# Performance work log

Hardware: AMD Instinct MI355X
Metric: run time of the kernel (lower is better)

Reference implementation:

```python
import jax, jax.numpy as jnp
import numpy as np

M = 65536  # total flattened feature length (sum of ragged segment lengths n_k)
K = 4096   # number of segments (sub-networks)
B = 256    # batch size


def setup_inputs() -> dict:
    key = jax.random.key(0)
    k1, k2, k3 = jax.random.split(key, 3)
    x = jax.random.normal(k1, (B, 1, M), dtype=jnp.float32)
    w = jax.random.normal(k2, (M,), dtype=jnp.float32)
    # contiguous ragged segments: sorted segment ids in [0, K)
    seg_ids = jnp.sort(jax.random.randint(k3, (M,), 0, K, dtype=jnp.int32))
    return {"x": x, "w": w, "seg_ids": seg_ids, "num_segments": K}


def reference(x, w, seg_ids, num_segments):
    # GINN input layer: for each batch row, slice the flat input into K ragged
    # contiguous segments, dot each segment with the matching slice of the flat
    # weight vector, concatenate the K scalars, apply tanh.
    # Equivalent fused form: u2[b,k] = sum_{i in seg k} w[i]*x[b,0,i]; out = tanh(u2)
    xs = x[:, 0, :]                      # [B, M]
    prod = xs * w                        # [B, M] elementwise
    seg_sum = jax.vmap(
        lambda p: jax.ops.segment_sum(p, seg_ids, num_segments=num_segments)
    )(prod)                              # [B, K]
    return jnp.tanh(seg_sum)
```

## Files before the change

kernel.cpp:

```cpp
#include <hip/hip_runtime.h>


#define TPB   256
#define WIN   1024
#define EPL   16
#define SLOTS 192
#define ITERS 4

__global__ __launch_bounds__(TPB) void zero_out_k(float* __restrict__ out, int n4) {
    int i = blockIdx.x * blockDim.x + threadIdx.x;
    if (i < n4) reinterpret_cast<float4*>(out)[i] = make_float4(0.f, 0.f, 0.f, 0.f);
}

__global__ __launch_bounds__(TPB) void seg_persist(
        const float* __restrict__ x,
        const float* __restrict__ w,
        const int*   __restrict__ ids,
        float* __restrict__ out,
        float* __restrict__ carry,
        int M, int K, int NW, int B) {
    __shared__ float slab[TPB / 64][2][SLOTS];

    const int ln  = threadIdx.x & 63;
    const int wv  = threadIdx.x >> 6;
    const int wid = blockIdx.x * (TPB / 64) + wv;
    const int win = wid % NW;
    const int grp = wid / NW;
    const int bp0 = grp * ITERS;
    const size_t mbase = (size_t)win * WIN + (size_t)ln * EPL;
    const int halfB = B / 2;

    const int4*   id4 = reinterpret_cast<const int4*>(ids + mbase);
    const float4* w4  = reinterpret_cast<const float4*>(w + mbase);
    int4   i0 = id4[0], i1 = id4[1], i2 = id4[2], i3 = id4[3];
    float4 q0 = w4[0],  q1 = w4[1],  q2 = w4[2],  q3 = w4[3];

    const int firstId = __shfl(i0.x, 0);
    const int lastId  = __shfl(i3.w, 63);
    const int span    = min(lastId - firstId + 1, SLOTS);

    float* __restrict__ sA = slab[wv][0];
    float* __restrict__ sB = slab[wv][1];

    float4 aC[4], cC[4], aN[4], cN[4];
    {
        const float4* xa4 = reinterpret_cast<const float4*>(x + (size_t)bp0 * M + mbase);
        const float4* xb4 = reinterpret_cast<const float4*>(x + (size_t)(bp0 + halfB) * M + mbase);
        aC[0] = xa4[0]; aC[1] = xa4[1]; aC[2] = xa4[2]; aC[3] = xa4[3];
        cC[0] = xb4[0]; cC[1] = xb4[1]; cC[2] = xb4[2]; cC[3] = xb4[3];
    }

    #pragma unroll
    for (int it = 0; it < ITERS; ++it) {
        const int bp  = bp0 + it;
        const int bpn = bp0 + ((it + 1 < ITERS) ? (it + 1) : it);
        {
            const float4* xa4 = reinterpret_cast<const float4*>(x + (size_t)bpn * M + mbase);
            const float4* xb4 = reinterpret_cast<const float4*>(x + (size_t)(bpn + halfB) * M + mbase);
            aN[0] = xa4[0]; aN[1] = xa4[1]; aN[2] = xa4[2]; aN[3] = xa4[3];
            cN[0] = xb4[0]; cN[1] = xb4[1]; cN[2] = xb4[2]; cN[3] = xb4[3];
        }
        #pragma unroll
        for (int i = ln; i < 2 * SLOTS; i += 64) (&sA[0])[i] = 0.f;
        asm volatile("s_waitcnt lgkmcnt(0)" ::: "memory");
        __builtin_amdgcn_sched_barrier(0);

        float accA = 0.f, accB = 0.f;
        int prev = i0.x;
        #define STEP(idv, xav, xbv, wvv)                               \
            if ((idv) != prev) {                                       \
                int s = min(prev - firstId, SLOTS - 1);                \
                atomicAdd(&sA[s], accA);                               \
                atomicAdd(&sB[s], accB);                               \
                accA = 0.f; accB = 0.f; prev = (idv);                  \
            }                                                          \
            accA = fmaf((xav), (wvv), accA);                           \
            accB = fmaf((xbv), (wvv), accB);

        STEP(i0.x, aC[0].x, cC[0].x, q0.x)  STEP(i0.y, aC[0].y, cC[0].y, q0.y)
        STEP(i0.z, aC[0].z, cC[0].z, q0.z)  STEP(i0.w, aC[0].w, cC[0].w, q0.w)
        STEP(i1.x, aC[1].x, cC[1].x, q1.x)  STEP(i1.y, aC[1].y, cC[1].y, q1.y)
        STEP(i1.z, aC[1].z, cC[1].z, q1.z)  STEP(i1.w, aC[1].w, cC[1].w, q1.w)
        STEP(i2.x, aC[2].x, cC[2].x, q2.x)  STEP(i2.y, aC[2].y, cC[2].y, q2.y)
        STEP(i2.z, aC[2].z, cC[2].z, q2.z)  STEP(i2.w, aC[2].w, cC[2].w, q2.w)
        STEP(i3.x, aC[3].x, cC[3].x, q3.x)  STEP(i3.y, aC[3].y, cC[3].y, q3.y)
        STEP(i3.z, aC[3].z, cC[3].z, q3.z)  STEP(i3.w, aC[3].w, cC[3].w, q3.w)
        #undef STEP
        {
            int s = min(prev - firstId, SLOTS - 1);
            atomicAdd(&sA[s], accA);
            atomicAdd(&sB[s], accB);
        }
        asm volatile("s_waitcnt lgkmcnt(0)" ::: "memory");
        __builtin_amdgcn_sched_barrier(0);

        for (int i = ln; i < 2 * span; i += 64) {
            int rr  = (i >= span) ? 1 : 0;
            int s   = i - rr * span;
            int id  = firstId + s;
            int row = rr ? (bp + halfB) : bp;
            float v = slab[wv][rr][s];
            if (s == 0)
                carry[((size_t)row * NW + win) * 2 + 0] = v;
            else if (id == lastId)
                carry[((size_t)row * NW + win) * 2 + 1] = v;
            else
                out[(size_t)row * K + id] = tanhf(v);
        }
        asm volatile("s_waitcnt lgkmcnt(0)" ::: "memory");
        __builtin_amdgcn_sched_barrier(0);

        #pragma unroll
        for (int j = 0; j < 4; ++j) { aC[j] = aN[j]; cC[j] = cN[j]; }
    }
}

__global__ __launch_bounds__(TPB) void seg_fixup(
        const int*   __restrict__ ids,
        const float* __restrict__ carry,
        float* __restrict__ out,
        int K, int NW, int B) {
    int t = blockIdx.x * blockDim.x + threadIdx.x;
    if (t >= B * NW) return;
    int row = t / NW;
    int win = t - row * NW;

    int firstId = ids[win * WIN];
    int lastId  = ids[win * WIN + WIN - 1];
    float cF = carry[((size_t)row * NW + win) * 2 + 0];
    float cL = carry[((size_t)row * NW + win) * 2 + 1];

    int prevLast = (win > 0) ? ids[win * WIN - 1] : -1;
    if (prevLast != firstId)
        out[(size_t)row * K + firstId] = tanhf(cF);

    float tot = cL;
    if (win + 1 < NW) {
        int nextFirst = ids[(win + 1) * WIN];
        if (nextFirst == lastId)
            tot += carry[((size_t)row * NW + win + 1) * 2 + 0];
    }
    out[(size_t)row * K + lastId] = tanhf(tot);
}

extern "C" void kernel_launch(void* const* d_in, const int* in_sizes, int n_in,
                              void* d_out, int out_size, void* d_ws, size_t ws_size,
                              hipStream_t stream) {
    const float* x       = (const float*)d_in[0];
    const float* w       = (const float*)d_in[1];
    const int*   seg_ids = (const int*)d_in[2];
    float* out = (float*)d_out;

    const int M = in_sizes[1];
    const int B = in_sizes[0] / M;
    const int K = out_size / B;
    const int NW = M / WIN;

    float* carry = (float*)d_ws;

    const int n4 = out_size / 4;
    zero_out_k<<<(n4 + TPB - 1) / TPB, TPB, 0, stream>>>(out, n4);

    const int nwaves = NW * ((B / 2) / ITERS);
    const int nblk   = nwaves / (TPB / 64);
    seg_persist<<<nblk, TPB, 0, stream>>>(x, w, seg_ids, out, carry, M, K, NW, B);

    const int nfix = B * NW;
    seg_fixup<<<(nfix + TPB - 1) / TPB, TPB, 0, stream>>>(seg_ids, carry, out, K, NW, B);
}
```

Measured before the change: 31.24 us.

## Stage x through LDS with direct global-to-LDS loads and drop zero kernel

Replaces the persistent per-wave kernel, which prefetched x into registers over four iterations, with a 2D grid of one block per window and eight batch rows. x is copied straight into LDS using global_load_lds, and each wave reduces two rows. The separate output-zeroing kernel is removed; the fixup kernel now zeroes the empty segment ids between windows instead. This saves a launch and register pressure, but loses the cross-iteration prefetch overlap and reloads ids and w in every block.

```diff
diff --git a/kernel.cpp b/kernel.cpp
--- a/kernel.cpp
+++ b/kernel.cpp
@@ -3,115 +3,113 @@
 
 #define TPB   256
 #define WIN   1024
-#define EPL   16
+#define ROWS  8
 #define SLOTS 192
-#define ITERS 4
 
-__global__ __launch_bounds__(TPB) void zero_out_k(float* __restrict__ out, int n4) {
-    int i = blockIdx.x * blockDim.x + threadIdx.x;
-    if (i < n4) reinterpret_cast<float4*>(out)[i] = make_float4(0.f, 0.f, 0.f, 0.f);
+__device__ __forceinline__ void gload_lds16(const float* g, void* l) {
+    __builtin_amdgcn_global_load_lds(
+        (const __attribute__((address_space(1))) void*)g,
+        (__attribute__((address_space(3)))  void*)l,
+        16, 0, 0);
 }
 
-__global__ __launch_bounds__(TPB) void seg_persist(
+__global__ __launch_bounds__(TPB) void seg_glds(
         const float* __restrict__ x,
         const float* __restrict__ w,
         const int*   __restrict__ ids,
         float* __restrict__ out,
         float* __restrict__ carry,
-        int M, int K, int NW, int B) {
-    __shared__ float slab[TPB / 64][2][SLOTS];
+        int M, int K, int NW) {
+    __shared__ float4 xstage[ROWS][WIN / 4];
+    __shared__ float  slab[ROWS][SLOTS];
 
-    const int ln  = threadIdx.x & 63;
-    const int wv  = threadIdx.x >> 6;
-    const int wid = blockIdx.x * (TPB / 64) + wv;
-    const int win = wid % NW;
-    const int grp = wid / NW;
-    const int bp0 = grp * ITERS;
-    const size_t mbase = (size_t)win * WIN + (size_t)ln * EPL;
-    const int halfB = B / 2;
+    const int ln   = threadIdx.x & 63;
+    const int wv   = threadIdx.x >> 6;
+    const int win  = blockIdx.x;
+    const int r0   = blockIdx.y * ROWS;
+    const int rowA = r0 + 2 * wv;
+    const int rowB = rowA + 1;
+    const int fb   = win * WIN + ln * 4;
 
-    const int4*   id4 = reinterpret_cast<const int4*>(ids + mbase);
-    const float4* w4  = reinterpret_cast<const float4*>(w + mbase);
-    int4   i0 = id4[0], i1 = id4[1], i2 = id4[2], i3 = id4[3];
-    float4 q0 = w4[0],  q1 = w4[1],  q2 = w4[2],  q3 = w4[3];
+    const float* ga = x + (size_t)rowA * M + fb;
+    const float* gb = x + (size_t)rowB * M + fb;
+    #pragma unroll
+    for (int j = 0; j < 4; ++j)
+        gload_lds16(ga + j * 256, (void*)&xstage[2 * wv + 0][j * 64]);
+    #pragma unroll
+    for (int j = 0; j < 4; ++j)
+        gload_lds16(gb + j * 256, (void*)&xstage[2 * wv + 1][j * 64]);
+
+    int4   i0 = *reinterpret_cast<const int4*>(ids + fb);
+    int4   i1 = *reinterpret_cast<const int4*>(ids + fb + 256);
+    int4   i2 = *reinterpret_cast<const int4*>(ids + fb + 512);
+    int4   i3 = *reinterpret_cast<const int4*>(ids + fb + 768);
+    float4 q0 = *reinterpret_cast<const float4*>(w + fb);
+    float4 q1 = *reinterpret_cast<const float4*>(w + fb + 256);
+    float4 q2 = *reinterpret_cast<const float4*>(w + fb + 512);
+    float4 q3 = *reinterpret_cast<const float4*>(w + fb + 768);
+
+    #pragma unroll
+    for (int i = ln; i < 2 * SLOTS; i += 64)
+        (&slab[2 * wv][0])[i] = 0.f;
+
+    asm volatile("s_waitcnt vmcnt(0) lgkmcnt(0)" ::: "memory");
+    __builtin_amdgcn_sched_barrier(0);
 
     const int firstId = __shfl(i0.x, 0);
     const int lastId  = __shfl(i3.w, 63);
     const int span    = min(lastId - firstId + 1, SLOTS);
 
-    float* __restrict__ sA = slab[wv][0];
-    float* __restrict__ sB = slab[wv][1];
-
-    float4 aC[4], cC[4], aN[4], cN[4];
-    {
-        const float4* xa4 = reinterpret_cast<const float4*>(x + (size_t)bp0 * M + mbase);
-        const float4* xb4 = reinterpret_cast<const float4*>(x + (size_t)(bp0 + halfB) * M + mbase);
-        aC[0] = xa4[0]; aC[1] = xa4[1]; aC[2] = xa4[2]; aC[3] = xa4[3];
-        cC[0] = xb4[0]; cC[1] = xb4[1]; cC[2] = xb4[2]; cC[3] = xb4[3];
+    #pragma unroll
+    for (int rr = 0; rr < 2; ++rr) {
+        float* __restrict__ sl = slab[2 * wv + rr];
+        float acc = 0.f;
+        int prev = i0.x;
+        #define STEP(idv, xv, wvv)                                     \
+            if ((idv) != prev) {                                       \
+                atomicAdd(&sl[min(prev - firstId, SLOTS - 1)], acc);   \
+                acc = 0.f; prev = (idv);                               \
+            }                                                          \
+            acc = fmaf((xv), (wvv), acc);
+        {
+            float4 xq = xstage[2 * wv + rr][0 * 64 + ln];
+            STEP(i0.x, xq.x, q0.x) STEP(i0.y, xq.y, q0.y)
+            STEP(i0.z, xq.z, q0.z) STEP(i0.w, xq.w, q0.w)
+        }
+        {
+            float4 xq = xstage[2 * wv + rr][1 * 64 + ln];
+            STEP(i1.x, xq.x, q1.x) STEP(i1.y, xq.y, q1.y)
+            STEP(i1.z, xq.z, q1.z) STEP(i1.w, xq.w, q1.w)
+        }
+        {
+            float4 xq = xstage[2 * wv + rr][2 * 64 + ln];
+            STEP(i2.x, xq.x, q2.x) STEP(i2.y, xq.y, q2.y)
+            STEP(i2.z, xq.z, q2.z) STEP(i2.w, xq.w, q2.w)
+        }
+        {
+            float4 xq = xstage[2 * wv + rr][3 * 64 + ln];
+            STEP(i3.x, xq.x, q3.x) STEP(i3.y, xq.y, q3.y)
+            STEP(i3.z, xq.z, q3.z) STEP(i3.w, xq.w, q3.w)
+        }
+        #undef STEP
+        atomicAdd(&sl[min(prev - firstId, SLOTS - 1)], acc);
     }
 
-    #pragma unroll
-    for (int it = 0; it < ITERS; ++it) {
-        const int bp  = bp0 + it;
-        const int bpn = bp0 + ((it + 1 < ITERS) ? (it + 1) : it);
-        {
-            const float4* xa4 = reinterpret_cast<const float4*>(x + (size_t)bpn * M + mbase);
-            const float4* xb4 = reinterpret_cast<const float4*>(x + (size_t)(bpn + halfB) * M + mbase);
-            aN[0] = xa4[0]; aN[1] = xa4[1]; aN[2] = xa4[2]; aN[3] = xa4[3];
-            cN[0] = xb4[0]; cN[1] = xb4[1]; cN[2] = xb4[2]; cN[3] = xb4[3];
-        }
-        #pragma unroll
-        for (int i = ln; i < 2 * SLOTS; i += 64) (&sA[0])[i] = 0.f;
-        asm volatile("s_waitcnt lgkmcnt(0)" ::: "memory");
-        __builtin_amdgcn_sched_barrier(0);
+    asm volatile("s_waitcnt lgkmcnt(0)" ::: "memory");
+    __builtin_amdgcn_sched_barrier(0);
 
-        float accA = 0.f, accB = 0.f;
-        int prev = i0.x;
-        #define STEP(idv, xav, xbv, wvv)                               \
-            if ((idv) != prev) {                                       \
-                int s = min(prev - firstId, SLOTS - 1);                \
-                atomicAdd(&sA[s], accA);                               \
-                atomicAdd(&sB[s], accB);                               \
-                accA = 0.f; accB = 0.f; prev = (idv);                  \
-            }                                                          \
-            accA = fmaf((xav), (wvv), accA);                           \
-            accB = fmaf((xbv), (wvv), accB);
-
-        STEP(i0.x, aC[0].x, cC[0].x, q0.x)  STEP(i0.y, aC[0].y, cC[0].y, q0.y)
-        STEP(i0.z, aC[0].z, cC[0].z, q0.z)  STEP(i0.w, aC[0].w, cC[0].w, q0.w)
-        STEP(i1.x, aC[1].x, cC[1].x, q1.x)  STEP(i1.y, aC[1].y, cC[1].y, q1.y)
-        STEP(i1.z, aC[1].z, cC[1].z, q1.z)  STEP(i1.w, aC[1].w, cC[1].w, q1.w)
-        STEP(i2.x, aC[2].x, cC[2].x, q2.x)  STEP(i2.y, aC[2].y, cC[2].y, q2.y)
-        STEP(i2.z, aC[2].z, cC[2].z, q2.z)  STEP(i2.w, aC[2].w, cC[2].w, q2.w)
-        STEP(i3.x, aC[3].x, cC[3].x, q3.x)  STEP(i3.y, aC[3].y, cC[3].y, q3.y)
-        STEP(i3.z, aC[3].z, cC[3].z, q3.z)  STEP(i3.w, aC[3].w, cC[3].w, q3.w)
-        #undef STEP
-        {
-            int s = min(prev - firstId, SLOTS - 1);
-            atomicAdd(&sA[s], accA);
-            atomicAdd(&sB[s], accB);
-        }
-        asm volatile("s_waitcnt lgkmcnt(0)" ::: "memory");
-        __builtin_amdgcn_sched_barrier(0);
-
-        for (int i = ln; i < 2 * span; i += 64) {
-            int rr  = (i >= span) ? 1 : 0;
-            int s   = i - rr * span;
-            int id  = firstId + s;
-            int row = rr ? (bp + halfB) : bp;
-            float v = slab[wv][rr][s];
-            if (s == 0)
-                carry[((size_t)row * NW + win) * 2 + 0] = v;
-            else if (id == lastId)
-                carry[((size_t)row * NW + win) * 2 + 1] = v;
-            else
-                out[(size_t)row * K + id] = tanhf(v);
-        }
-        asm volatile("s_waitcnt lgkmcnt(0)" ::: "memory");
-        __builtin_amdgcn_sched_barrier(0);
-
-        #pragma unroll
-        for (int j = 0; j < 4; ++j) { aC[j] = aN[j]; cC[j] = cN[j]; }
+    for (int i = ln; i < 2 * span; i += 64) {
+        int rr  = (i >= span) ? 1 : 0;
+        int s   = i - rr * span;
+        int id  = firstId + s;
+        int row = rr ? rowB : rowA;
+        float v = slab[2 * wv + rr][s];
+        if (s == 0)
+            carry[((size_t)row * NW + win) * 2 + 0] = v;
+        else if (id == lastId)
+            carry[((size_t)row * NW + win) * 2 + 1] = v;
+        else
+            out[(size_t)row * K + id] = tanhf(v);
     }
 }
 
@@ -134,13 +132,17 @@
     if (prevLast != firstId)
         out[(size_t)row * K + firstId] = tanhf(cF);
 
+    int nextFirst = (win + 1 < NW) ? ids[(win + 1) * WIN] : K;
     float tot = cL;
-    if (win + 1 < NW) {
-        int nextFirst = ids[(win + 1) * WIN];
-        if (nextFirst == lastId)
-            tot += carry[((size_t)row * NW + win + 1) * 2 + 0];
-    }
+    if (nextFirst == lastId)
+        tot += carry[((size_t)row * NW + win + 1) * 2 + 0];
     out[(size_t)row * K + lastId] = tanhf(tot);
+
+    for (int id = lastId + 1; id < nextFirst; ++id)
+        out[(size_t)row * K + id] = 0.f;
+    if (win == 0)
+        for (int id = 0; id < firstId; ++id)
+            out[(size_t)row * K + id] = 0.f;
 }
 
 extern "C" void kernel_launch(void* const* d_in, const int* in_sizes, int n_in,
@@ -158,12 +160,8 @@
 
     float* carry = (float*)d_ws;
 
-    const int n4 = out_size / 4;
-    zero_out_k<<<(n4 + TPB - 1) / TPB, TPB, 0, stream>>>(out, n4);
-
-    const int nwaves = NW * ((B / 2) / ITERS);
-    const int nblk   = nwaves / (TPB / 64);
-    seg_persist<<<nblk, TPB, 0, stream>>>(x, w, seg_ids, out, carry, M, K, NW, B);
+    dim3 grid(NW, B / ROWS);
+    seg_glds<<<grid, TPB, 0, stream>>>(x, w, seg_ids, out, carry, M, K, NW);
 
     const int nfix = B * NW;
     seg_fixup<<<(nfix + TPB - 1) / TPB, TPB, 0, stream>>>(seg_ids, carry, out, K, NW, B);
```

After: 44.75 us. +43.2%, slower.
